# Kernel optimization log

Hardware: AMD Instinct MI355X
Metric: run time of the kernel (lower is better)

The kernel has to match this reference:

```python
import jax, jax.numpy as jnp
import numpy as np

BATCH, SEQ, IN, HID = 32, 1024, 512, 1024


def setup_inputs() -> dict:
    key = jax.random.key(0)
    std = 1.0 / np.sqrt(HID)
    ks = jax.random.split(key, 16)
    u = lambda k, shape: jax.random.uniform(k, shape, jnp.float32, -std, std)
    return {
        "x": jax.random.normal(ks[0], (BATCH, SEQ, IN), jnp.float32),
        "Wi": u(ks[1], (IN, 2 * HID)),
        "Wh": u(ks[2], (HID, 2 * HID)),
        "B": u(ks[3], (2 * HID,)),
        "Wni": u(ks[4], (IN, HID)),
        "Wnh": u(ks[5], (HID, HID)),
        "Bni": u(ks[6], (HID,)),
        "Bnh": u(ks[7], (HID,)),
        "Winvi": u(ks[8], (IN, 2 * HID)),
        "Winvh": u(ks[9], (HID, 2 * HID)),
        "Binv": u(ks[10], (2 * HID,)),
        "Wninvi": u(ks[11], (IN, HID)),
        "Wninvh": u(ks[12], (HID, HID)),
        "Bninvi": u(ks[13], (HID,)),
        "Bninvh": u(ks[14], (HID,)),
    }


def _gru_scan(x, Wi, Wh, Bg, Wni, Wnh, Bni, Bnh, reverse):
    # x: [B,S,I]; precompute input projections once (same math, batched GEMM)
    H = Wnh.shape[0]
    gi = jnp.einsum('bsi,ig->bsg', x, Wi) + Bg   # [B,S,2H]
    ni = jnp.einsum('bsi,ih->bsh', x, Wni) + Bni # [B,S,H]
    h0 = jnp.zeros((x.shape[0], H), x.dtype)

    def step(h, inp):
        g_t, n_t = inp                        # [B,2H], [B,H]
        gates = g_t + h @ Wh
        r = jax.nn.sigmoid(gates[:, :H])
        z = jax.nn.sigmoid(gates[:, H:])
        n = jnp.tanh(n_t + r * (h @ Wnh + Bnh))
        h = (1 - z) * n + z * h
        return h, h

    hT, hs = jax.lax.scan(step, h0, (gi.swapaxes(0, 1), ni.swapaxes(0, 1)),
                          reverse=reverse)
    return hs.swapaxes(0, 1), hT              # [B,S,H], [B,H]


def reference(x, Wi, Wh, B, Wni, Wnh, Bni, Bnh,
              Winvi, Winvh, Binv, Wninvi, Wninvh, Bninvi, Bninvh):
    out_f, h_f = _gru_scan(x, Wi, Wh, B, Wni, Wnh, Bni, Bnh, reverse=False)
    out_b, h_b = _gru_scan(x, Winvi, Winvh, Binv, Wninvi, Wninvh, Bninvi, Bninvh,
                           reverse=True)
    output = jnp.concatenate([out_f, out_b], axis=-1)  # [B,S,2H]
    ht = jnp.concatenate([h_f, h_b], axis=-1)          # [B,2H]
    return output, ht
```

## Files before the change

kernel.cpp:

```cpp
#include <hip/hip_runtime.h>
#include <cstdint>
#include <cstddef>

typedef __attribute__((ext_vector_type(8))) short s8v;
typedef __attribute__((ext_vector_type(4))) float f4v;
typedef __attribute__((ext_vector_type(4))) unsigned int u4v;

#define DEVFN __device__ __forceinline__

DEVFN unsigned short f2bf(float f) {
    unsigned int u = __builtin_bit_cast(unsigned int, f);
    return (unsigned short)((u + 0x7FFFu + ((u >> 16) & 1u)) >> 16);
}
DEVFN float bf2f(unsigned short h) {
    unsigned int u = ((unsigned int)h) << 16;
    return __builtin_bit_cast(float, u);
}
DEVFN float sigm(float x) { return 1.0f / (1.0f + __expf(-x)); }
DEVFN float tanh_fast(float x) { float e = __expf(2.0f * x); return 1.0f - 2.0f / (e + 1.0f); }

DEVFN u4v pack8(const unsigned short o[8]) {
    u4v v;
    v[0] = (unsigned)o[0] | ((unsigned)o[1] << 16);
    v[1] = (unsigned)o[2] | ((unsigned)o[3] << 16);
    v[2] = (unsigned)o[4] | ((unsigned)o[5] << 16);
    v[3] = (unsigned)o[6] | ((unsigned)o[7] << 16);
    return v;
}

DEVFN void store_wt(unsigned int* p, unsigned int v) {
    asm volatile("global_store_dword %0, %1, off sc0 sc1"
                 :: "v"(p), "v"(v) : "memory");
}
DEVFN unsigned poll_load(const unsigned int* p) {
    unsigned v;
    asm volatile("global_load_dword %0, %1, off sc0 sc1\n\t"
                 "s_waitcnt vmcnt(0)"
                 : "=v"(v) : "v"(p) : "memory");
    return v;
}
DEVFN void gather_h(const void* p0, const void* p1,
                    u4v& a0, u4v& a1, u4v& a2, u4v& a3,
                    u4v& a4, u4v& a5, u4v& a6, u4v& a7) {
    asm volatile(
        "global_load_dwordx4 %0, %8, off sc0 sc1\n\t"
        "global_load_dwordx4 %1, %8, off offset:1024 sc0 sc1\n\t"
        "global_load_dwordx4 %2, %8, off offset:2048 sc0 sc1\n\t"
        "global_load_dwordx4 %3, %8, off offset:3072 sc0 sc1\n\t"
        "global_load_dwordx4 %4, %9, off sc0 sc1\n\t"
        "global_load_dwordx4 %5, %9, off offset:1024 sc0 sc1\n\t"
        "global_load_dwordx4 %6, %9, off offset:2048 sc0 sc1\n\t"
        "global_load_dwordx4 %7, %9, off offset:3072 sc0 sc1\n\t"
        "s_waitcnt vmcnt(0)"
        : "=&v"(a0), "=&v"(a1), "=&v"(a2), "=&v"(a3),
          "=&v"(a4), "=&v"(a5), "=&v"(a6), "=&v"(a7)
        : "v"(p0), "v"(p1)
        : "memory");
}

constexpr int BB = 32, SS = 1024, II = 512, HH = 1024;
constexpr int NCOL = 6144;

constexpr size_t OFF_X    = 0;
constexpr size_t SZ_X     = (size_t)BB * SS * II * 2;
constexpr size_t OFF_WINT = OFF_X + SZ_X;
constexpr size_t SZ_WINT  = (size_t)NCOL * II * 2;
constexpr size_t OFF_WREC = OFF_WINT + SZ_WINT;
constexpr size_t SZ_WREC  = (size_t)2 * 3072 * HH * 2;
constexpr size_t OFF_BIAS = OFF_WREC + SZ_WREC;
constexpr size_t SZ_BIAS  = (size_t)NCOL * 4;
constexpr size_t OFF_H    = OFF_BIAS + SZ_BIAS;
constexpr size_t SZ_H     = (size_t)2 * 2 * 2 * 64 * 512;
constexpr size_t OFF_BAR  = OFF_H + SZ_H;
constexpr size_t SZ_BAR   = 4096;
constexpr size_t OFF_G    = OFF_BAR + SZ_BAR;
constexpr size_t SZ_G     = (size_t)SS * BB * NCOL * 2;
constexpr size_t WS_NEED  = OFF_G + SZ_G;

constexpr int WL_OFF = 0;
constexpr int PL_OFF = 98304;
constexpr int GR_OFF = 124416;
constexpr int PF_OFF = 130560;
constexpr int RD_OFF = 130592;
constexpr int PG_OFF = 130608;
constexpr int SMEM_TOT = 130624;
constexpr int PLF = 4 * 3 * 16 * 17;

__global__ void prep_kernel(
    const float* __restrict__ x,
    const float* __restrict__ Wi, const float* __restrict__ Wni,
    const float* __restrict__ Winvi, const float* __restrict__ Wninvi,
    const float* __restrict__ Wh, const float* __restrict__ Wnh,
    const float* __restrict__ Winvh, const float* __restrict__ Wninvh,
    const float* __restrict__ Bg, const float* __restrict__ Bni,
    const float* __restrict__ Binv, const float* __restrict__ Bninvi,
    unsigned short* __restrict__ xb, unsigned short* __restrict__ WinT,
    unsigned short* __restrict__ Wrec, float* __restrict__ bias)
{
    constexpr int NX8  = (BB * SS * II) / 8;
    constexpr int NWI8 = (NCOL * II) / 8;
    constexpr int NWR8 = (2 * 3072 * HH) / 8;
    constexpr int TOT  = NX8 + NWI8 + NWR8 + NCOL;
    for (int i = blockIdx.x * blockDim.x + threadIdx.x; i < TOT;
         i += gridDim.x * blockDim.x) {
        if (i < NX8) {
            const float* sp = x + (size_t)i * 8;
            unsigned short o[8];
#pragma unroll
            for (int j = 0; j < 8; ++j) o[j] = f2bf(sp[j]);
            *(u4v*)(xb + (size_t)i * 8) = pack8(o);
        } else if (i < NX8 + NWI8) {
            int u = i - NX8;
            int n = u >> 6, k0 = (u & 63) * 8;
            const float* src; int stride;
            if (n < 2048)      { src = Wi + n;            stride = 2048; }
            else if (n < 3072) { src = Wni + (n - 2048);  stride = 1024; }
            else if (n < 5120) { src = Winvi + (n - 3072); stride = 2048; }
            else               { src = Wninvi + (n - 5120); stride = 1024; }
            unsigned short o[8];
#pragma unroll
            for (int j = 0; j < 8; ++j) o[j] = f2bf(src[(size_t)(k0 + j) * stride]);
            *(u4v*)(WinT + (size_t)n * 512 + k0) = pack8(o);
        } else if (i < NX8 + NWI8 + NWR8) {
            int u = i - NX8 - NWI8;
            int R = u >> 7, k0 = (u & 127) * 8;
            int dir = R / 3072, n = R % 3072;
            const float* src; int stride;
            if (n < 2048) { src = (dir ? Winvh : Wh) + n;          stride = 2048; }
            else          { src = (dir ? Wninvh : Wnh) + (n - 2048); stride = 1024; }
            unsigned short o[8];
#pragma unroll
            for (int j = 0; j < 8; ++j) o[j] = f2bf(src[(size_t)(k0 + j) * stride]);
            *(u4v*)(Wrec + (size_t)R * 1024 + k0) = pack8(o);
        } else {
            int c = i - NX8 - NWI8 - NWR8;
            int dir = c / 3072, cc = c % 3072;
            bias[c] = (cc < 2048) ? (dir ? Binv : Bg)[cc]
                                  : (dir ? Bninvi : Bni)[cc - 2048];
        }
    }
}

#define GLL16(gp, lp) __builtin_amdgcn_global_load_lds( \
    (const __attribute__((address_space(1))) void*)(gp), \
    (__attribute__((address_space(3))) void*)(lp), 16, 0, 0)

__global__ __launch_bounds__(256, 2) void gemm_in(
    const unsigned short* __restrict__ xb,
    const unsigned short* __restrict__ WinT,
    const float* __restrict__ bias,
    unsigned short* __restrict__ G)
{
    __shared__ char smem[32768];
    char* As = smem;
    char* Bs = smem + 16384;
    const int tid = threadIdx.x, lane = tid & 63, wid = tid >> 6;
    int wg = blockIdx.x;
    int swz = (wg & 7) * 1536 + (wg >> 3);
    const int m0 = (swz & 255) * 128, n0 = (swz >> 8) * 128;
    const int l15 = lane & 15, hi = lane >> 4;
    const int mw = (wid & 1) * 64, nw = (wid >> 1) * 64;

    f4v acc[4][4] = {};

    const char* xrow = (const char*)xb;
    const char* wrow = (const char*)WinT;

    for (int kt = 0; kt < 8; ++kt) {
        const int kb0 = kt * 128;
#pragma unroll
        for (int r = 0; r < 4; ++r) {
            int q = wid * 4 + r;
            int o = q * 1024 + lane * 16;
            int row = o >> 7;
            int kbs = (o ^ ((row & 7) << 4)) & 127;
            GLL16(xrow + (size_t)(m0 + row) * 1024 + kb0 + kbs, As + q * 1024);
            GLL16(wrow + (size_t)(n0 + row) * 1024 + kb0 + kbs, Bs + q * 1024);
        }
        __syncthreads();
#pragma unroll
        for (int kc = 0; kc < 2; ++kc) {
            s8v a[4], b[4];
#pragma unroll
            for (int mt = 0; mt < 4; ++mt) {
                int row = mw + mt * 16 + l15;
                int off = (row << 7) + kc * 64 + hi * 16;
                a[mt] = *(const s8v*)(As + (off ^ ((row & 7) << 4)));
            }
#pragma unroll
            for (int nt = 0; nt < 4; ++nt) {
                int row = nw + nt * 16 + l15;
                int off = (row << 7) + kc * 64 + hi * 16;
                b[nt] = *(const s8v*)(Bs + (off ^ ((row & 7) << 4)));
            }
#pragma unroll
            for (int mt = 0; mt < 4; ++mt)
#pragma unroll
                for (int nt = 0; nt < 4; ++nt)
                    acc[mt][nt] = __builtin_amdgcn_mfma_f32_16x16x32_bf16(
                        a[mt], b[nt], acc[mt][nt], 0, 0, 0);
        }
        __syncthreads();
    }
#pragma unroll
    for (int mt = 0; mt < 4; ++mt) {
#pragma unroll
        for (int rg = 0; rg < 4; ++rg) {
            int m = m0 + mw + mt * 16 + hi * 4 + rg;
            int bi = m >> 10, si = m & 1023;
            int bg = bi >> 4, b16 = bi & 15;
#pragma unroll
            for (int nt = 0; nt < 4; ++nt) {
                int n = n0 + nw + nt * 16 + l15;
                int dir = (n >= 3072);
                int rem = n - dir * 3072;
                int gate = rem >> 10, col = rem & 1023;
                int jg = col >> 4, j = col & 15;
                size_t idx = (((((size_t)si * 2 + dir) * 64 + jg) * 2 + bg) * 16
                              + b16) * 48 + gate * 16 + j;
                G[idx] = f2bf(acc[mt][nt][rg] + bias[n]);
            }
        }
    }
}

__global__ __launch_bounds__(320, 1) void gru_rec(
    const unsigned short* __restrict__ G,
    const unsigned short* __restrict__ Wrec,
    const float* __restrict__ Bnh,
    const float* __restrict__ Bninvh,
    unsigned short* __restrict__ hbuf,
    float* __restrict__ out,
    unsigned int* __restrict__ flags)
{
    extern __shared__ char smem[];
    char* wl = smem + WL_OFF;
    float* pl = (float*)(smem + PL_OFF);
    unsigned short* gring = (unsigned short*)(smem + GR_OFF);
    volatile int* pflag = (volatile int*)(smem + PF_OFF);
    volatile int* gready = (volatile int*)(smem + RD_OFF);
    volatile int* gprog  = (volatile int*)(smem + PG_OFF);

    const int tid = threadIdx.x, lane = tid & 63, wid = tid >> 6;
    const int bid = blockIdx.x;
    const int dir = bid >> 7, bg = (bid >> 6) & 1, jg = bid & 63;
    const int jbase = jg * 16, bb = bg * 16;
    const int l15 = lane & 15, hi = lane >> 4;
    unsigned int* fl = flags + ((dir * 2 + bg) << 8);

    if (tid < 4) { gready[tid] = -1; gprog[tid] = -1; }
    if (tid >= 4 && tid < 12) pflag[tid - 4] = -1;
    if (tid < 256) {
        const char* wsrc = (const char*)Wrec;
        for (int q = 0; q < 24; ++q) {
            int o = (q * 256 + tid) * 16;
            int c = o >> 11;
            int kb = (o ^ ((c & 7) << 4)) & 2047;
            int n = dir * 3072 + (c >> 4) * 1024 + jbase + (c & 15);
            *(u4v*)(wl + o) = *(const u4v*)(wsrc + (size_t)n * 2048 + kb);
        }
    }
    const int b_l = tid >> 4, j_l = tid & 15;
    const float bnh = (dir ? Bninvh : Bnh)[jbase + (j_l & 15)];
    __syncthreads();

    const size_t gstride_b = (size_t)2 * 64 * 2 * 768 * 2;
    const char* gcb = (const char*)G + (((size_t)dir * 64 + jg) * 2 + bg) * 1536;

    if (wid == 4) {
        char* grb = (char*)gring;
        for (int t = 0; t < 1024; ++t) {
            const int slot = t & 3;
            if (t >= 4) {
                int v;
                do { v = gprog[lane & 3]; } while (!__all(v >= t - 4));
            }
            const int gpos = dir ? (1023 - t) : t;
            const char* src = gcb + (size_t)gpos * gstride_b + lane * 32;
            if (lane < 48) {
                u4v d0 = *(const u4v*)(src);
                u4v d1 = *(const u4v*)(src + 16);
                *(u4v*)(grb + slot * 1536 + lane * 32) = d0;
                *(u4v*)(grb + slot * 1536 + lane * 32 + 16) = d1;
            }
            asm volatile("s_waitcnt lgkmcnt(0) vmcnt(0)" ::: "memory");
            if (lane == 0) gready[slot] = t;
        }
        return;
    }

    float h_old = 0.0f;
    unsigned int* hbuf32 = (unsigned int*)hbuf;

    for (int s = 0; s < 1024; ++s) {
        const int par = s & 1;
        float* plc = pl + par * PLF;

        const int slot = s & 3;
        {
            int r;
            do { r = gready[slot]; } while (r != s);
        }
        asm volatile("" ::: "memory");
        const int gb = slot * 768 + b_l * 48 + j_l;
        unsigned short gr = gring[gb];
        unsigned short gz = gring[gb + 16];
        unsigned short gn = gring[gb + 32];
        asm volatile("s_waitcnt lgkmcnt(0)" ::: "memory");
        if (lane == 0) gprog[wid] = s;

        float rsum = 0.f, zsum = 0.f, nsum = 0.f;
        if (s > 0) {
            const unsigned tgt = (unsigned)s;
            const unsigned int* fp = fl + wid * 64 + lane;
            unsigned v;
            do { v = poll_load(fp); } while (!__all(v >= tgt));

            const int rbuf = par ^ 1;
            const char* hb = (const char*)hbuf +
                ((((size_t)(dir * 2 + rbuf) * 2 + bg) * 64)
                 + (size_t)(wid * 16 + (hi >> 1))) * 512
                + l15 * 32 + (hi & 1) * 16;
            u4v u[8];
            gather_h(hb, hb + 4096, u[0], u[1], u[2], u[3],
                     u[4], u[5], u[6], u[7]);

            f4v acc[3] = {};
#pragma unroll
            for (int p = 0; p < 3; ++p) {
                int c = p * 16 + l15;
                int cbase = c << 11;
                int sw = (c & 7) << 4;
#pragma unroll
                for (int kc = 0; kc < 8; ++kc) {
                    int off = cbase + (wid << 9) + kc * 64 + hi * 16;
                    s8v bf = *(const s8v*)(wl + (off ^ sw));
                    acc[p] = __builtin_amdgcn_mfma_f32_16x16x32_bf16(
                        __builtin_bit_cast(s8v, u[kc]), bf, acc[p], 0, 0, 0);
                }
            }
#pragma unroll
            for (int p = 0; p < 3; ++p)
#pragma unroll
                for (int rg = 0; rg < 4; ++rg)
                    plc[((wid * 3 + p) * 16 + hi * 4 + rg) * 17 + l15] = acc[p][rg];
            asm volatile("s_waitcnt lgkmcnt(0)" ::: "memory");
            if (lane == 0) pflag[par * 4 + wid] = s;

            {
                int f0, f1, f2, f3;
                do {
                    f0 = pflag[par * 4 + 0]; f1 = pflag[par * 4 + 1];
                    f2 = pflag[par * 4 + 2]; f3 = pflag[par * 4 + 3];
                } while (f0 < s || f1 < s || f2 < s || f3 < s);
            }
            asm volatile("" ::: "memory");
#pragma unroll
            for (int w = 0; w < 4; ++w) {
                rsum += plc[((w * 3 + 0) * 16 + b_l) * 17 + j_l];
                zsum += plc[((w * 3 + 1) * 16 + b_l) * 17 + j_l];
                nsum += plc[((w * 3 + 2) * 16 + b_l) * 17 + j_l];
            }
        }

        float rv = sigm(rsum + bf2f(gr));
        float zv = sigm(zsum + bf2f(gz));
        float nv = tanh_fast(bf2f(gn) + rv * (nsum + bnh));
        float hn = (1.0f - zv) * nv + zv * h_old;
        h_old = hn;

        if (s < 1023) {
            unsigned short hbv = f2bf(hn);
            unsigned int other = (unsigned int)(unsigned short)__shfl_xor((int)hbv, 1);
            if (!(tid & 1)) {
                size_t w32 = ((((size_t)(dir * 2 + par) * 2 + bg) * 64 + jg) * 128)
                             + b_l * 8 + (j_l >> 1);
                store_wt(hbuf32 + w32, (unsigned)hbv | (other << 16));
            }
        }
        const int s_out = dir ? (1023 - s) : s;
        out[((size_t)(bb + b_l) * SS + s_out) * 2048 + dir * 1024 + jbase + j_l] = hn;
        if (s == 1023)
            out[(size_t)BB * SS * 2048 + (size_t)(bb + b_l) * 2048 +
                dir * 1024 + jbase + j_l] = hn;

        if (s < 1023) {
            asm volatile("s_waitcnt vmcnt(0)" ::: "memory");
            if (lane == 0)
                store_wt(&fl[jg * 4 + wid], (unsigned)(s + 1));
        }
    }
}

extern "C" void kernel_launch(void* const* d_in, const int* in_sizes, int n_in,
                              void* d_out, int out_size, void* d_ws, size_t ws_size,
                              hipStream_t stream)
{
    if (n_in < 15) return;
    const float* x      = (const float*)d_in[0];
    const float* Wi     = (const float*)d_in[1];
    const float* Wh     = (const float*)d_in[2];
    const float* Bg     = (const float*)d_in[3];
    const float* Wni    = (const float*)d_in[4];
    const float* Wnh    = (const float*)d_in[5];
    const float* Bni    = (const float*)d_in[6];
    const float* Bnh    = (const float*)d_in[7];
    const float* Winvi  = (const float*)d_in[8];
    const float* Winvh  = (const float*)d_in[9];
    const float* Binv   = (const float*)d_in[10];
    const float* Wninvi = (const float*)d_in[11];
    const float* Wninvh = (const float*)d_in[12];
    const float* Bninvi = (const float*)d_in[13];
    const float* Bninvh = (const float*)d_in[14];

    if (ws_size < WS_NEED) {
        hipMemsetAsync(d_out, 0, (size_t)out_size * 4, stream);
        return;
    }
    char* ws = (char*)d_ws;
    unsigned short* xb   = (unsigned short*)(ws + OFF_X);
    unsigned short* WinT = (unsigned short*)(ws + OFF_WINT);
    unsigned short* Wrec = (unsigned short*)(ws + OFF_WREC);
    float*          bias = (float*)(ws + OFF_BIAS);
    unsigned short* hbuf = (unsigned short*)(ws + OFF_H);
    unsigned int*   bar  = (unsigned int*)(ws + OFF_BAR);
    unsigned short* G    = (unsigned short*)(ws + OFF_G);

    hipMemsetAsync(ws + OFF_BAR, 0, SZ_BAR, stream);

    prep_kernel<<<4096, 256, 0, stream>>>(
        x, Wi, Wni, Winvi, Wninvi, Wh, Wnh, Winvh, Wninvh,
        Bg, Bni, Binv, Bninvi, xb, WinT, Wrec, bias);

    gemm_in<<<12288, 256, 0, stream>>>(xb, WinT, bias, G);

    hipFuncSetAttribute(reinterpret_cast<const void*>(&gru_rec),
                        hipFuncAttributeMaxDynamicSharedMemorySize, SMEM_TOT);
    gru_rec<<<256, 320, SMEM_TOT, stream>>>(
        G, Wrec, Bnh, Bninvh, hbuf, (float*)d_out, bar);
}
```

Baseline: 3.837 ms.

## Replace flag handshake with step-tagged hidden-state data and ring-buffered progress

```diff
diff --git a/kernel.cpp b/kernel.cpp
--- a/kernel.cpp
+++ b/kernel.cpp
@@ -39,22 +39,38 @@
                  : "=v"(v) : "v"(p) : "memory");
     return v;
 }
-DEVFN void gather_h(const void* p0, const void* p1,
-                    u4v& a0, u4v& a1, u4v& a2, u4v& a3,
-                    u4v& a4, u4v& a5, u4v& a6, u4v& a7) {
+DEVFN void gather_tagged(const void* b0, const void* b1, const void* b2,
+                         const void* b3, const void* pp,
+                         u4v& g0, u4v& g1, u4v& g2, u4v& g3,
+                         u4v& g4, u4v& g5, u4v& g6, u4v& g7,
+                         u4v& g8, u4v& g9, u4v& g10, u4v& g11,
+                         u4v& g12, u4v& g13, u4v& g14, u4v& g15,
+                         unsigned& pv) {
     asm volatile(
-        "global_load_dwordx4 %0, %8, off sc0 sc1\n\t"
-        "global_load_dwordx4 %1, %8, off offset:1024 sc0 sc1\n\t"
-        "global_load_dwordx4 %2, %8, off offset:2048 sc0 sc1\n\t"
-        "global_load_dwordx4 %3, %8, off offset:3072 sc0 sc1\n\t"
-        "global_load_dwordx4 %4, %9, off sc0 sc1\n\t"
-        "global_load_dwordx4 %5, %9, off offset:1024 sc0 sc1\n\t"
-        "global_load_dwordx4 %6, %9, off offset:2048 sc0 sc1\n\t"
-        "global_load_dwordx4 %7, %9, off offset:3072 sc0 sc1\n\t"
+        "global_load_dwordx4 %0, %17, off sc0 sc1\n\t"
+        "global_load_dwordx4 %1, %17, off offset:16 sc0 sc1\n\t"
+        "global_load_dwordx4 %2, %17, off offset:2048 sc0 sc1\n\t"
+        "global_load_dwordx4 %3, %17, off offset:2064 sc0 sc1\n\t"
+        "global_load_dwordx4 %4, %18, off sc0 sc1\n\t"
+        "global_load_dwordx4 %5, %18, off offset:16 sc0 sc1\n\t"
+        "global_load_dwordx4 %6, %18, off offset:2048 sc0 sc1\n\t"
+        "global_load_dwordx4 %7, %18, off offset:2064 sc0 sc1\n\t"
+        "global_load_dwordx4 %8, %19, off sc0 sc1\n\t"
+        "global_load_dwordx4 %9, %19, off offset:16 sc0 sc1\n\t"
+        "global_load_dwordx4 %10, %19, off offset:2048 sc0 sc1\n\t"
+        "global_load_dwordx4 %11, %19, off offset:2064 sc0 sc1\n\t"
+        "global_load_dwordx4 %12, %20, off sc0 sc1\n\t"
+        "global_load_dwordx4 %13, %20, off offset:16 sc0 sc1\n\t"
+        "global_load_dwordx4 %14, %20, off offset:2048 sc0 sc1\n\t"
+        "global_load_dwordx4 %15, %20, off offset:2064 sc0 sc1\n\t"
+        "global_load_dword %16, %21, off sc0 sc1\n\t"
         "s_waitcnt vmcnt(0)"
-        : "=&v"(a0), "=&v"(a1), "=&v"(a2), "=&v"(a3),
-          "=&v"(a4), "=&v"(a5), "=&v"(a6), "=&v"(a7)
-        : "v"(p0), "v"(p1)
+        : "=&v"(g0), "=&v"(g1), "=&v"(g2), "=&v"(g3),
+          "=&v"(g4), "=&v"(g5), "=&v"(g6), "=&v"(g7),
+          "=&v"(g8), "=&v"(g9), "=&v"(g10), "=&v"(g11),
+          "=&v"(g12), "=&v"(g13), "=&v"(g14), "=&v"(g15),
+          "=&v"(pv)
+        : "v"(b0), "v"(b1), "v"(b2), "v"(b3), "v"(pp)
         : "memory");
 }
 
@@ -70,7 +86,7 @@
 constexpr size_t OFF_BIAS = OFF_WREC + SZ_WREC;
 constexpr size_t SZ_BIAS  = (size_t)NCOL * 4;
 constexpr size_t OFF_H    = OFF_BIAS + SZ_BIAS;
-constexpr size_t SZ_H     = (size_t)2 * 2 * 2 * 64 * 512;
+constexpr size_t SZ_H     = (size_t)4 * 4 * 64 * 1024;
 constexpr size_t OFF_BAR  = OFF_H + SZ_H;
 constexpr size_t SZ_BAR   = 4096;
 constexpr size_t OFF_G    = OFF_BAR + SZ_BAR;
@@ -224,14 +240,21 @@
     }
 }
 
+#define UNPACK8(dst, A, B) { u4v d_;                                   \
+    d_[0] = __builtin_amdgcn_perm(A[1], A[0], 0x05040100u);            \
+    d_[1] = __builtin_amdgcn_perm(A[3], A[2], 0x05040100u);            \
+    d_[2] = __builtin_amdgcn_perm(B[1], B[0], 0x05040100u);            \
+    d_[3] = __builtin_amdgcn_perm(B[3], B[2], 0x05040100u);            \
+    dst = __builtin_bit_cast(s8v, d_); }
+
 __global__ __launch_bounds__(320, 1) void gru_rec(
     const unsigned short* __restrict__ G,
     const unsigned short* __restrict__ Wrec,
     const float* __restrict__ Bnh,
     const float* __restrict__ Bninvh,
-    unsigned short* __restrict__ hbuf,
+    unsigned int* __restrict__ hbuf32,
     float* __restrict__ out,
-    unsigned int* __restrict__ flags)
+    unsigned int* __restrict__ prog)
 {
     extern __shared__ char smem[];
     char* wl = smem + WL_OFF;
@@ -244,9 +267,9 @@
     const int tid = threadIdx.x, lane = tid & 63, wid = tid >> 6;
     const int bid = blockIdx.x;
     const int dir = bid >> 7, bg = (bid >> 6) & 1, jg = bid & 63;
+    const int grp = dir * 2 + bg;
     const int jbase = jg * 16, bb = bg * 16;
     const int l15 = lane & 15, hi = lane >> 4;
-    unsigned int* fl = flags + ((dir * 2 + bg) << 8);
 
     if (tid < 4) { gready[tid] = -1; gprog[tid] = -1; }
     if (tid >= 4 && tid < 12) pflag[tid - 4] = -1;
@@ -290,7 +313,12 @@
     }
 
     float h_old = 0.0f;
-    unsigned int* hbuf32 = (unsigned int*)hbuf;
+
+    const char* hregion = (const char*)hbuf32;
+    const unsigned int* pp = prog + ((size_t)grp * 64 + lane) * 4 + (jg >> 4);
+    unsigned int* ppub = prog + ((size_t)grp * 64 + jg) * 4 + wid;
+    unsigned int* hstore_base = hbuf32 + (size_t)grp * 4 * 64 * 256
+                                + (size_t)jg * 256 + b_l * 16 + j_l;
 
     for (int s = 0; s < 1024; ++s) {
         const int par = s & 1;
@@ -310,20 +338,35 @@
         if (lane == 0) gprog[wid] = s;
 
         float rsum = 0.f, zsum = 0.f, nsum = 0.f;
+        unsigned pv = 0;
+
         if (s > 0) {
-            const unsigned tgt = (unsigned)s;
-            const unsigned int* fp = fl + wid * 64 + lane;
-            unsigned v;
-            do { v = poll_load(fp); } while (!__all(v >= tgt));
-
-            const int rbuf = par ^ 1;
-            const char* hb = (const char*)hbuf +
-                ((((size_t)(dir * 2 + rbuf) * 2 + bg) * 64)
-                 + (size_t)(wid * 16 + (hi >> 1))) * 512
-                + l15 * 32 + (hi & 1) * 16;
-            u4v u[8];
-            gather_h(hb, hb + 4096, u[0], u[1], u[2], u[3],
-                     u[4], u[5], u[6], u[7]);
+            const int rbuf = (s - 1) & 3;
+            const char* hb = hregion
+                + ((size_t)(grp * 4 + rbuf) * 64 + wid * 16) * 1024
+                + (size_t)(hi >> 1) * 1024 + l15 * 64 + (hi & 1) * 32;
+            const unsigned tagpat = (unsigned)(s - 1) << 16;
+            u4v tp; tp[0] = tagpat; tp[1] = tagpat; tp[2] = tagpat; tp[3] = tagpat;
+            u4v g0, g1, g2, g3, g4, g5, g6, g7,
+                g8, g9, g10, g11, g12, g13, g14, g15;
+            for (;;) {
+                gather_tagged(hb, hb + 4096, hb + 8192, hb + 12288, pp,
+                              g0, g1, g2, g3, g4, g5, g6, g7,
+                              g8, g9, g10, g11, g12, g13, g14, g15, pv);
+                u4v a = (g0 ^ tp) | (g1 ^ tp) | (g2 ^ tp) | (g3 ^ tp)
+                      | (g4 ^ tp) | (g5 ^ tp) | (g6 ^ tp) | (g7 ^ tp)
+                      | (g8 ^ tp) | (g9 ^ tp) | (g10 ^ tp) | (g11 ^ tp)
+                      | (g12 ^ tp) | (g13 ^ tp) | (g14 ^ tp) | (g15 ^ tp);
+                unsigned bad = (a[0] | a[1] | a[2] | a[3]) & 0xffff0000u;
+                if (__all(bad == 0)) break;
+            }
+            if (lane == 0) store_wt(ppub, (unsigned)s);
+
+            s8v af[8];
+            UNPACK8(af[0], g0, g1);   UNPACK8(af[1], g2, g3);
+            UNPACK8(af[2], g4, g5);   UNPACK8(af[3], g6, g7);
+            UNPACK8(af[4], g8, g9);   UNPACK8(af[5], g10, g11);
+            UNPACK8(af[6], g12, g13); UNPACK8(af[7], g14, g15);
 
             f4v acc[3] = {};
 #pragma unroll
@@ -336,7 +379,7 @@
                     int off = cbase + (wid << 9) + kc * 64 + hi * 16;
                     s8v bf = *(const s8v*)(wl + (off ^ sw));
                     acc[p] = __builtin_amdgcn_mfma_f32_16x16x32_bf16(
-                        __builtin_bit_cast(s8v, u[kc]), bf, acc[p], 0, 0, 0);
+                        af[kc], bf, acc[p], 0, 0, 0);
                 }
             }
 #pragma unroll
@@ -370,25 +413,17 @@
         h_old = hn;
 
         if (s < 1023) {
-            unsigned short hbv = f2bf(hn);
-            unsigned int other = (unsigned int)(unsigned short)__shfl_xor((int)hbv, 1);
-            if (!(tid & 1)) {
-                size_t w32 = ((((size_t)(dir * 2 + par) * 2 + bg) * 64 + jg) * 128)
-                             + b_l * 8 + (j_l >> 1);
-                store_wt(hbuf32 + w32, (unsigned)hbv | (other << 16));
-            }
+            if (s >= 4) {
+                while (!__all((int)pv >= s - 3)) pv = poll_load(pp);
+            }
+            unsigned val = ((unsigned)s << 16) | (unsigned)f2bf(hn);
+            store_wt(hstore_base + (size_t)(s & 3) * 64 * 256, val);
         }
         const int s_out = dir ? (1023 - s) : s;
         out[((size_t)(bb + b_l) * SS + s_out) * 2048 + dir * 1024 + jbase + j_l] = hn;
         if (s == 1023)
             out[(size_t)BB * SS * 2048 + (size_t)(bb + b_l) * 2048 +
                 dir * 1024 + jbase + j_l] = hn;
-
-        if (s < 1023) {
-            asm volatile("s_waitcnt vmcnt(0)" ::: "memory");
-            if (lane == 0)
-                store_wt(&fl[jg * 4 + wid], (unsigned)(s + 1));
-        }
     }
 }
 
@@ -422,7 +457,7 @@
     unsigned short* WinT = (unsigned short*)(ws + OFF_WINT);
     unsigned short* Wrec = (unsigned short*)(ws + OFF_WREC);
     float*          bias = (float*)(ws + OFF_BIAS);
-    unsigned short* hbuf = (unsigned short*)(ws + OFF_H);
+    unsigned int*   hbuf = (unsigned int*)(ws + OFF_H);
     unsigned int*   bar  = (unsigned int*)(ws + OFF_BAR);
     unsigned short* G    = (unsigned short*)(ws + OFF_G);
 
```

Measured after the change: 8.295 ms. 2.16x slower.
